# Kernel optimization log

Measured on AMD Instinct MI355X. Metric: run time of the kernel, lower is better.

Reference implementation:

```python
import jax, jax.numpy as jnp
import numpy as np

N_TOKENS = 7168
EMBED_DIM = 256
N_HEADS = 8
HEAD_DIM = EMBED_DIM // N_HEADS  # 32
HALF = HEAD_DIM // 2             # 16 rotary frequency pairs per head
BATCH = 4
MAX_LEN = 2048
POSITION_DIM = 2
N_LEVELS = 4
LN_EPS = 1e-5
SPATIAL_THETA = 100.0
LEVEL_THETA = 10.0


def setup_inputs() -> dict:
    key = jax.random.key(0)
    ks = jax.random.split(key, 6)
    x = jax.random.normal(ks[0], (N_TOKENS, EMBED_DIM), jnp.float32)
    level_indices = jax.random.randint(ks[1], (N_TOKENS,), 0, N_LEVELS, dtype=jnp.int32)
    level_spatial_shapes = jnp.array([[32, 32], [16, 16], [8, 8], [4, 4]], jnp.int32)
    # positions in each token's own level coordinate space
    u = jax.random.uniform(ks[2], (N_TOKENS, POSITION_DIM), jnp.float32)
    spatial_positions = u * level_spatial_shapes[level_indices].astype(jnp.float32)
    # ragged batch boundaries: lengths [2048, 1536, 2048, 1536]
    batch_offsets = jnp.array([0, 2048, 3584, 5632, 7168], jnp.int32)
    ln_w = jnp.ones((EMBED_DIM,), jnp.float32)
    ln_b = jnp.zeros((EMBED_DIM,), jnp.float32)
    qkv_w = jax.random.normal(ks[3], (3 * EMBED_DIM, EMBED_DIM), jnp.float32) * (EMBED_DIM ** -0.5)
    out_w = jax.random.normal(ks[4], (EMBED_DIM, EMBED_DIM), jnp.float32) * (EMBED_DIM ** -0.5)
    # ND-RoPE frequencies: (position_dim+1, n_heads, head_dim//2).
    # Spatial dims share magnitude theta_s^(-i/HALF) split over a random per-head
    # direction angle; level dim uses theta_l^(-i/HALF).
    mag_s = SPATIAL_THETA ** (-jnp.arange(HALF, dtype=jnp.float32) / HALF)
    mag_l = LEVEL_THETA ** (-jnp.arange(HALF, dtype=jnp.float32) / HALF)
    phi = jax.random.uniform(ks[5], (N_HEADS, HALF), jnp.float32) * (2.0 * jnp.pi)
    freqs = jnp.stack([mag_s * jnp.cos(phi),
                       mag_s * jnp.sin(phi),
                       jnp.broadcast_to(mag_l, (N_HEADS, HALF))], axis=0)
    return {"x": x, "spatial_positions": spatial_positions,
            "level_indices": level_indices, "level_spatial_shapes": level_spatial_shapes,
            "batch_offsets": batch_offsets, "ln_w": ln_w, "ln_b": ln_b,
            "qkv_w": qkv_w, "out_w": out_w, "freqs": freqs}


def reference(x, spatial_positions, level_indices, level_spatial_shapes,
              batch_offsets, ln_w, ln_b, qkv_w, out_w, freqs):
    residual = x
    # pre-norm LayerNorm
    mu = jnp.mean(x, -1, keepdims=True)
    var = jnp.mean((x - mu) ** 2, -1, keepdims=True)
    xn = (x - mu) * jax.lax.rsqrt(var + LN_EPS) * ln_w + ln_b
    q, k, v = jnp.split(xn @ qkv_w.T, 3, axis=-1)  # each (N, E)
    # prep_multilevel_positions: rescale each level to the max level's coordinate
    # frame and append the level index as an extra position dim.
    shapes_tok = level_spatial_shapes[level_indices].astype(jnp.float32)  # (N, 2)
    max_shape = jnp.max(level_spatial_shapes, axis=0).astype(jnp.float32)  # (2,)
    pos = jnp.concatenate([spatial_positions * (max_shape / shapes_tok),
                           level_indices[:, None].astype(jnp.float32)], axis=-1)  # (N, 3)
    # per-head ND RoPE: angle = sum_d pos_d * freq_d
    theta = jnp.einsum('nd,dhf->nhf', pos, freqs)  # (N, H, HALF)
    cos, sin = jnp.cos(theta), jnp.sin(theta)

    def rope(t):
        t = t.reshape(N_TOKENS, N_HEADS, HALF, 2)
        r = jnp.stack([t[..., 0] * cos - t[..., 1] * sin,
                       t[..., 0] * sin + t[..., 1] * cos], axis=-1)
        return r.reshape(N_TOKENS, EMBED_DIM)

    q, k = rope(q), rope(k)
    # concatenated -> padded (B, S, E)
    tok = jnp.arange(N_TOKENS)
    b_of = jnp.searchsorted(batch_offsets, tok, side='right') - 1  # (N,) batch index
    p_of = tok - batch_offsets[b_of]                               # (N,) pos in batch
    lens = batch_offsets[1:] - batch_offsets[:-1]
    pad_mask = jnp.arange(MAX_LEN)[None, :] >= lens[:, None]  # (B, S), True = padding

    def heads(t):
        padded = jnp.zeros((BATCH, MAX_LEN, EMBED_DIM), t.dtype).at[b_of, p_of].set(t)
        return padded.reshape(BATCH, MAX_LEN, N_HEADS, HEAD_DIM).transpose(0, 2, 1, 3)

    qh, kh, vh = heads(q), heads(k), heads(v)  # (B, H, S, hd)
    scores = jnp.einsum('bhqd,bhkd->bhqk', qh, kh) / np.float32(np.sqrt(HEAD_DIM))
    scores = jnp.where(pad_mask[:, None, None, :], jnp.float32(-1e9), scores)
    attn = jax.nn.softmax(scores, axis=-1)
    out = jnp.einsum('bhqk,bhkd->bhqd', attn, vh)
    out = out.transpose(0, 2, 1, 3).reshape(BATCH, MAX_LEN, EMBED_DIM)
    out_cat = out[b_of, p_of]  # padded -> concatenated (padded rows dropped)
    return out_cat @ out_w.T + residual
```

## Files before the change

kernel.cpp:

```cpp
#include <hip/hip_runtime.h>
#include <hip/hip_bf16.h>

#define NT   7168
#define ED   256
#define NH   8
#define HD   32
#define HF   16
#define QKVN 768
#define QSCL 0.25503471600819466f

typedef float f32x4  __attribute__((ext_vector_type(4)));
typedef __bf16 bf16x8 __attribute__((ext_vector_type(8)));

__device__ __forceinline__ short f2bf(float f) {
    union { float f; unsigned u; } v; v.f = f;
    unsigned r = v.u + 0x7FFFu + ((v.u >> 16) & 1u);
    return (short)(r >> 16);
}
__device__ __forceinline__ float fexp2(float x) {
    float r; asm("v_exp_f32 %0, %1" : "=v"(r) : "v"(x)); return r;
}
__device__ __forceinline__ unsigned cvtpk(float lo, float hi) {
    unsigned r; asm("v_cvt_pk_bf16_f32 %0, %1, %2" : "=v"(r) : "v"(lo), "v"(hi)); return r;
}
__device__ __forceinline__ float bf2f(short s) {
    union { unsigned u; float f; } v; v.u = ((unsigned)(unsigned short)s) << 16;
    return v.f;
}
__device__ __forceinline__ unsigned pack2bf(float a, float b) {
    union { float f; unsigned u; } ua, ub; ua.f = a; ub.f = b;
    return ((ua.u + 0x8000u) >> 16) | ((ub.u + 0x8000u) & 0xFFFF0000u);
}
__device__ __forceinline__ void gll16(const void* g, void* l) {
    __builtin_amdgcn_global_load_lds((const __attribute__((address_space(1))) void*)g,
                                     (__attribute__((address_space(3))) void*)l, 16, 0, 0);
}

__global__ __launch_bounds__(256) void ln_conv_kernel(const float* __restrict__ x,
                                                      const float* __restrict__ w,
                                                      const float* __restrict__ b,
                                                      short* __restrict__ xn,
                                                      const float* __restrict__ qkvw,
                                                      const float* __restrict__ outw,
                                                      short* __restrict__ wq,
                                                      short* __restrict__ wo,
                                                      const float* __restrict__ sp,
                                                      const int* __restrict__ lvl,
                                                      const int* __restrict__ shp,
                                                      const float* __restrict__ freqs,
                                                      unsigned* __restrict__ tab) {
    int bid = blockIdx.x;
    int tid = threadIdx.x;
    if (bid >= NT / 4) {
        int i = (bid - NT / 4) * 256 + tid;
        if (i < QKVN * ED) wq[i] = f2bf(qkvw[i]);
        if (i < ED * ED)   wo[i] = f2bf(outw[i]);
        return;
    }
    int tok  = bid * 4 + (tid >> 6);
    int lane = tid & 63;
    const float4 xv = *reinterpret_cast<const float4*>(x + tok * ED + lane * 4);
    float s  = xv.x + xv.y + xv.z + xv.w;
    float ss = xv.x * xv.x + xv.y * xv.y + xv.z * xv.z + xv.w * xv.w;
#pragma unroll
    for (int m = 1; m < 64; m <<= 1) { s += __shfl_xor(s, m); ss += __shfl_xor(ss, m); }
    float mu  = s * (1.0f / ED);
    float inv = rsqrtf(ss * (1.0f / ED) - mu * mu + 1e-5f);
    const float4 wv = *reinterpret_cast<const float4*>(w + lane * 4);
    const float4 bv = *reinterpret_cast<const float4*>(b + lane * 4);
    short4 o;
    o.x = f2bf((xv.x - mu) * inv * wv.x + bv.x);
    o.y = f2bf((xv.y - mu) * inv * wv.y + bv.y);
    o.z = f2bf((xv.z - mu) * inv * wv.z + bv.z);
    o.w = f2bf((xv.w - mu) * inv * wv.w + bv.w);
    *reinterpret_cast<short4*>(xn + tok * ED + lane * 4) = o;

    int tt = bid * 4 + (tid >> 6);
    int h  = (tid >> 3) & 7;
    int f  = (tid & 7) * 2;
    int L = lvl[tt];
    float mx0 = fmaxf(fmaxf((float)shp[0], (float)shp[2]), fmaxf((float)shp[4], (float)shp[6]));
    float mx1 = fmaxf(fmaxf((float)shp[1], (float)shp[3]), fmaxf((float)shp[5], (float)shp[7]));
    float p0 = sp[tt * 2]     * (mx0 / (float)shp[L * 2]);
    float p1 = sp[tt * 2 + 1] * (mx1 / (float)shp[L * 2 + 1]);
    float p2 = (float)L;
    int fi = h * HF + f;
    float th0 = p0 * freqs[fi]       + p1 * freqs[128 + fi]       + p2 * freqs[256 + fi];
    float th1 = p0 * freqs[fi + 1]   + p1 * freqs[128 + fi + 1]   + p2 * freqs[256 + fi + 1];
    float sn0, cs0, sn1, cs1;
    __sincosf(th0, &sn0, &cs0);
    __sincosf(th1, &sn1, &cs1);
    uint2 pk;
    pk.x = pack2bf(cs0, sn0);
    pk.y = pack2bf(cs1, sn1);
    *reinterpret_cast<uint2*>(&tab[tt * 128 + fi]) = pk;
}

__global__ __launch_bounds__(256) void gemm_qkv(const short* __restrict__ A,
                                                const short* __restrict__ B,
                                                short* __restrict__ C,
                                                const unsigned* __restrict__ tab,
                                                short* __restrict__ vt) {
    int wv = threadIdx.x >> 6, lane = threadIdx.x & 63;
    int r = lane & 15, g = lane >> 4;
    int mt = blockIdx.x * 128 + wv * 32;
    int jt = blockIdx.y * 64;
    const short* arow0 = A + (mt + r) * ED + g * 8;
    const short* arow1 = A + (mt + 16 + r) * ED + g * 8;
    const short* brow  = B + (jt + r) * ED + g * 8;
    f32x4 acc0[4] = {{0,0,0,0},{0,0,0,0},{0,0,0,0},{0,0,0,0}};
    f32x4 acc1[4] = {{0,0,0,0},{0,0,0,0},{0,0,0,0},{0,0,0,0}};
#pragma unroll
    for (int k0 = 0; k0 < ED; k0 += 32) {
        bf16x8 a0 = *reinterpret_cast<const bf16x8*>(arow0 + k0);
        bf16x8 a1 = *reinterpret_cast<const bf16x8*>(arow1 + k0);
#pragma unroll
        for (int c = 0; c < 4; ++c) {
            bf16x8 bb = *reinterpret_cast<const bf16x8*>(brow + c * 16 * ED + k0);
            acc0[c] = __builtin_amdgcn_mfma_f32_16x16x32_bf16(a0, bb, acc0[c], 0, 0, 0);
            acc1[c] = __builtin_amdgcn_mfma_f32_16x16x32_bf16(a1, bb, acc1[c], 0, 0, 0);
        }
    }
    if (jt < 512) {
        const float qs = (jt < 256) ? QSCL : 1.0f;
        const int sgn = r & 1;
#pragma unroll
        for (int c = 0; c < 4; ++c) {
            int col = jt + c * 16 + r;
            int hf = ((col >> 5) & 7) * 16 + ((col >> 1) & 15);
#pragma unroll
            for (int rr = 0; rr < 4; ++rr) {
                int t0 = mt + g * 4 + rr;
                {
                    unsigned pk = tab[t0 * 128 + hf];
                    float cs = bf2f((short)(pk & 0xFFFF)), sn = bf2f((short)(pk >> 16));
                    float v = acc0[c][rr], p = __shfl_xor(v, 1);
                    float o = sgn ? (v * cs + p * sn) : (v * cs - p * sn);
                    C[t0 * QKVN + col] = f2bf(o * qs);
                }
                {
                    int t1 = t0 + 16;
                    unsigned pk = tab[t1 * 128 + hf];
                    float cs = bf2f((short)(pk & 0xFFFF)), sn = bf2f((short)(pk >> 16));
                    float v = acc1[c][rr], p = __shfl_xor(v, 1);
                    float o = sgn ? (v * cs + p * sn) : (v * cs - p * sn);
                    C[t1 * QKVN + col] = f2bf(o * qs);
                }
            }
        }
    } else {
#pragma unroll
        for (int c = 0; c < 4; ++c) {
            int dg = jt - 512 + c * 16 + r;
#pragma unroll
            for (int rr = 0; rr < 4; ++rr) {
                int t0 = mt + g * 4 + rr;
                int u0 = t0 & 63;
                int s0 = (u0 & 35) | ((u0 & 12) << 1) | ((u0 & 16) >> 2);
                vt[dg * NT + (t0 & ~63) + s0] = f2bf(acc0[c][rr]);
                int t1 = t0 + 16;
                int u1 = t1 & 63;
                int s1 = (u1 & 35) | ((u1 & 12) << 1) | ((u1 & 16) >> 2);
                vt[dg * NT + (t1 & ~63) + s1] = f2bf(acc1[c][rr]);
            }
        }
    }
}

__global__ __launch_bounds__(256) void gemm_out(const short* __restrict__ A,
                                                const short* __restrict__ B,
                                                const float* __restrict__ res,
                                                float* __restrict__ out) {
    int wv = threadIdx.x >> 6, lane = threadIdx.x & 63;
    int r = lane & 15, g = lane >> 4;
    int mt = blockIdx.x * 64 + wv * 16;
    int jt = blockIdx.y * 64;
    const short* arow = A + (mt + r) * ED + g * 8;
    const short* brow = B + (jt + r) * ED + g * 8;
    f32x4 acc[4] = {{0,0,0,0},{0,0,0,0},{0,0,0,0},{0,0,0,0}};
#pragma unroll
    for (int k0 = 0; k0 < ED; k0 += 32) {
        bf16x8 a = *reinterpret_cast<const bf16x8*>(arow + k0);
#pragma unroll
        for (int c = 0; c < 4; ++c) {
            bf16x8 bb = *reinterpret_cast<const bf16x8*>(brow + c * 16 * ED + k0);
            acc[c] = __builtin_amdgcn_mfma_f32_16x16x32_bf16(a, bb, acc[c], 0, 0, 0);
        }
    }
#pragma unroll
    for (int c = 0; c < 4; ++c)
#pragma unroll
        for (int rr = 0; rr < 4; ++rr) {
            int idx = (mt + g * 4 + rr) * ED + jt + c * 16 + r;
            out[idx] = acc[c][rr] + res[idx];
        }
}

__global__ __launch_bounds__(512) void attn_kernel(const short* __restrict__ qkv,
                                                   const short* __restrict__ vt,
                                                   short* __restrict__ obf) {
    __shared__ __align__(16) short smem[16384];
    const int tid = threadIdx.x;
    const int wv = tid >> 6, lane = tid & 63;
    const int bid = blockIdx.x;
    const int h = bid & 7, pr = bid >> 3;
    const int b = (pr >= 16) + (pr >= 28) + (pr >= 44);
    const int off = (b == 0) ? 0 : (b == 1) ? 2048 : (b == 2) ? 3584 : 5632;
    const int len = (b == 0) ? 2048 : (b == 1) ? 1536 : (b == 2) ? 2048 : 1536;
    const int pb  = (b == 0) ? 0 : (b == 1) ? 16 : (b == 2) ? 28 : 44;
    const int q0 = off + (pr - pb) * 128;
    const int r = lane & 15, g = lane >> 4;
    const int qi = wv & 3, half = wv >> 2;
    const int hl = len >> 1;
    const int nst = hl >> 6;
    const int qs = q0 + qi * 32;

    const int shalf = tid >> 8;
    const short* pK = qkv + ED + h * HD + (size_t)(off + ((tid & 255) >> 2)) * QKVN + (tid & 3) * 8;
    const short* pV = vt + (size_t)(h * HD + ((tid >> 2) & 31)) * NT + off + ((tid >> 7) & 1) * 32 + (tid & 3) * 8;
    const int hlK = hl * QKVN;
    const short* pKh = pK + (size_t)shalf * hlK;
    const short* pVh = pV + shalf * hl;

#define STAGE(B, s) { \
        gll16(pKh + (size_t)(s) * 64 * QKVN, &smem[(B) * 8192 +        tid * 8]); \
        gll16(pVh + (s) * 64,                &smem[(B) * 8192 + 4096 + tid * 8]); }

    bf16x8 qfA = *reinterpret_cast<const bf16x8*>(qkv + (size_t)(qs + r) * QKVN + h * HD + g * 8);
    bf16x8 qfB = *reinterpret_cast<const bf16x8*>(qkv + (size_t)(qs + 16 + r) * QKVN + h * HD + g * 8);
    union { unsigned u[4]; bf16x8 v; } onesu;
    onesu.u[0] = onesu.u[1] = onesu.u[2] = onesu.u[3] = 0x3F803F80u;
    const bf16x8 ones = onesu.v;

    f32x4 o0A = {0,0,0,0}, o1A = {0,0,0,0}, o0B = {0,0,0,0}, o1B = {0,0,0,0};
    f32x4 olA = {0,0,0,0}, olB = {0,0,0,0};

    STAGE(0, 0);
    __syncthreads();

    for (int st = 0; st < nst; ++st) {
        const int B = st & 1;
        if (st + 1 < nst) STAGE(B ^ 1, st + 1);
        const short* kl = &smem[B * 8192 + half * 2048];
        const short* vl = &smem[B * 8192 + 4096 + half * 2048];
        bf16x8 kf0 = *reinterpret_cast<const bf16x8*>(kl +        r * 32 + g * 8);
        bf16x8 kf1 = *reinterpret_cast<const bf16x8*>(kl +  512 + r * 32 + g * 8);
        bf16x8 kf2 = *reinterpret_cast<const bf16x8*>(kl + 1024 + r * 32 + g * 8);
        bf16x8 kf3 = *reinterpret_cast<const bf16x8*>(kl + 1536 + r * 32 + g * 8);
        bf16x8 v00 = *reinterpret_cast<const bf16x8*>(vl +        r * 32 + g * 8);
        bf16x8 v10 = *reinterpret_cast<const bf16x8*>(vl +  512 + r * 32 + g * 8);
        bf16x8 v01 = *reinterpret_cast<const bf16x8*>(vl + 1024 + r * 32 + g * 8);
        bf16x8 v11 = *reinterpret_cast<const bf16x8*>(vl + 1536 + r * 32 + g * 8);

        const f32x4 z = {0, 0, 0, 0};
        __builtin_amdgcn_s_setprio(1);
        f32x4 sA0 = __builtin_amdgcn_mfma_f32_16x16x32_bf16(kf0, qfA, z, 0, 0, 0);
        f32x4 sA1 = __builtin_amdgcn_mfma_f32_16x16x32_bf16(kf1, qfA, z, 0, 0, 0);
        f32x4 sA2 = __builtin_amdgcn_mfma_f32_16x16x32_bf16(kf2, qfA, z, 0, 0, 0);
        f32x4 sA3 = __builtin_amdgcn_mfma_f32_16x16x32_bf16(kf3, qfA, z, 0, 0, 0);
        f32x4 sB0 = __builtin_amdgcn_mfma_f32_16x16x32_bf16(kf0, qfB, z, 0, 0, 0);
        f32x4 sB1 = __builtin_amdgcn_mfma_f32_16x16x32_bf16(kf1, qfB, z, 0, 0, 0);
        f32x4 sB2 = __builtin_amdgcn_mfma_f32_16x16x32_bf16(kf2, qfB, z, 0, 0, 0);
        f32x4 sB3 = __builtin_amdgcn_mfma_f32_16x16x32_bf16(kf3, qfB, z, 0, 0, 0);
        __builtin_amdgcn_s_setprio(0);

#pragma unroll
        for (int i = 0; i < 4; ++i) {
            sA0[i] = fexp2(sA0[i]); sA1[i] = fexp2(sA1[i]);
            sA2[i] = fexp2(sA2[i]); sA3[i] = fexp2(sA3[i]);
            sB0[i] = fexp2(sB0[i]); sB1[i] = fexp2(sB1[i]);
            sB2[i] = fexp2(sB2[i]); sB3[i] = fexp2(sB3[i]);
        }
        union { unsigned u[4]; bf16x8 v; } pA0, pA1, pB0, pB1;
        pA0.u[0] = cvtpk(sA0[0], sA0[1]); pA0.u[1] = cvtpk(sA0[2], sA0[3]);
        pA0.u[2] = cvtpk(sA1[0], sA1[1]); pA0.u[3] = cvtpk(sA1[2], sA1[3]);
        pA1.u[0] = cvtpk(sA2[0], sA2[1]); pA1.u[1] = cvtpk(sA2[2], sA2[3]);
        pA1.u[2] = cvtpk(sA3[0], sA3[1]); pA1.u[3] = cvtpk(sA3[2], sA3[3]);
        pB0.u[0] = cvtpk(sB0[0], sB0[1]); pB0.u[1] = cvtpk(sB0[2], sB0[3]);
        pB0.u[2] = cvtpk(sB1[0], sB1[1]); pB0.u[3] = cvtpk(sB1[2], sB1[3]);
        pB1.u[0] = cvtpk(sB2[0], sB2[1]); pB1.u[1] = cvtpk(sB2[2], sB2[3]);
        pB1.u[2] = cvtpk(sB3[0], sB3[1]); pB1.u[3] = cvtpk(sB3[2], sB3[3]);
        __builtin_amdgcn_s_setprio(1);
        o0A = __builtin_amdgcn_mfma_f32_16x16x32_bf16(v00, pA0.v, o0A, 0, 0, 0);
        o0A = __builtin_amdgcn_mfma_f32_16x16x32_bf16(v01, pA1.v, o0A, 0, 0, 0);
        o1A = __builtin_amdgcn_mfma_f32_16x16x32_bf16(v10, pA0.v, o1A, 0, 0, 0);
        o1A = __builtin_amdgcn_mfma_f32_16x16x32_bf16(v11, pA1.v, o1A, 0, 0, 0);
        o0B = __builtin_amdgcn_mfma_f32_16x16x32_bf16(v00, pB0.v, o0B, 0, 0, 0);
        o0B = __builtin_amdgcn_mfma_f32_16x16x32_bf16(v01, pB1.v, o0B, 0, 0, 0);
        o1B = __builtin_amdgcn_mfma_f32_16x16x32_bf16(v10, pB0.v, o1B, 0, 0, 0);
        o1B = __builtin_amdgcn_mfma_f32_16x16x32_bf16(v11, pB1.v, o1B, 0, 0, 0);
        olA = __builtin_amdgcn_mfma_f32_16x16x32_bf16(ones, pA0.v, olA, 0, 0, 0);
        olA = __builtin_amdgcn_mfma_f32_16x16x32_bf16(ones, pA1.v, olA, 0, 0, 0);
        olB = __builtin_amdgcn_mfma_f32_16x16x32_bf16(ones, pB0.v, olB, 0, 0, 0);
        olB = __builtin_amdgcn_mfma_f32_16x16x32_bf16(ones, pB1.v, olB, 0, 0, 0);
        __builtin_amdgcn_s_setprio(0);
        __syncthreads();
    }

    float lA = olA[0], lB = olB[0];

    float* cf = (float*)smem + (qi * 64 + lane) * 19;
    if (half) {
#pragma unroll
        for (int i = 0; i < 4; ++i) {
            cf[i] = o0A[i]; cf[4 + i] = o1A[i]; cf[8 + i] = o0B[i]; cf[12 + i] = o1B[i];
        }
        cf[16] = lA; cf[17] = lB;
    }
    __syncthreads();
    if (!half) {
        lA += cf[16]; lB += cf[17];
#pragma unroll
        for (int i = 0; i < 4; ++i) {
            o0A[i] += cf[i];     o1A[i] += cf[4 + i];
            o0B[i] += cf[8 + i]; o1B[i] += cf[12 + i];
        }
        float iA = 1.f / lA, iB = 1.f / lB;
        short4 w;
        short* orowA = obf + (qs + r) * ED + h * HD;
        w.x = f2bf(o0A[0] * iA); w.y = f2bf(o0A[1] * iA);
        w.z = f2bf(o0A[2] * iA); w.w = f2bf(o0A[3] * iA);
        *reinterpret_cast<short4*>(orowA + g * 4) = w;
        w.x = f2bf(o1A[0] * iA); w.y = f2bf(o1A[1] * iA);
        w.z = f2bf(o1A[2] * iA); w.w = f2bf(o1A[3] * iA);
        *reinterpret_cast<short4*>(orowA + 16 + g * 4) = w;
        short* orowB = obf + (qs + 16 + r) * ED + h * HD;
        w.x = f2bf(o0B[0] * iB); w.y = f2bf(o0B[1] * iB);
        w.z = f2bf(o0B[2] * iB); w.w = f2bf(o0B[3] * iB);
        *reinterpret_cast<short4*>(orowB + g * 4) = w;
        w.x = f2bf(o1B[0] * iB); w.y = f2bf(o1B[1] * iB);
        w.z = f2bf(o1B[2] * iB); w.w = f2bf(o1B[3] * iB);
        *reinterpret_cast<short4*>(orowB + 16 + g * 4) = w;
    }
#undef STAGE
}

extern "C" void kernel_launch(void* const* d_in, const int* in_sizes, int n_in,
                              void* d_out, int out_size, void* d_ws, size_t ws_size,
                              hipStream_t stream) {
    const float* x     = (const float*)d_in[0];
    const float* sp    = (const float*)d_in[1];
    const int*   lvl   = (const int*)d_in[2];
    const int*   shp   = (const int*)d_in[3];
    const float* lnw   = (const float*)d_in[5];
    const float* lnb   = (const float*)d_in[6];
    const float* qkvw  = (const float*)d_in[7];
    const float* outw  = (const float*)d_in[8];
    const float* freqs = (const float*)d_in[9];
    float* out = (float*)d_out;

    char* ws = (char*)d_ws;
    short* xn  = (short*)ws; ws += NT * ED * 2;
    short* qkv = (short*)ws; ws += NT * QKVN * 2;
    short* vt  = (short*)ws; ws += ED * NT * 2;
    short* obf = (short*)ws; ws += NT * ED * 2;
    short* wq  = (short*)ws; ws += QKVN * ED * 2;
    short* wo  = (short*)ws; ws += ED * ED * 2;
    unsigned* tab = (unsigned*)ws; ws += NT * 128 * 4;

    ln_conv_kernel<<<dim3(NT / 4 + 768), dim3(256), 0, stream>>>(
        x, lnw, lnb, xn, qkvw, outw, wq, wo, sp, lvl, shp, freqs, tab);
    gemm_qkv<<<dim3(NT / 128, QKVN / 64), dim3(256), 0, stream>>>(xn, wq, qkv, tab, vt);
    attn_kernel<<<dim3(56 * 8), dim3(512), 0, stream>>>(qkv, vt, obf);
    gemm_out<<<dim3(NT / 64, ED / 64), dim3(256), 0, stream>>>(obf, wo, x, out);
}
```

Before: 67.51 us.

## Split attention key range four ways across 1024-thread blocks

The attention kernel now uses 16 waves per block instead of 8. Each query tile's key sequence is split into four quarters instead of two, with doubled shared memory for staging. The partial outputs and row sums from three waves are reduced through shared memory by the first quarter's wave. This is meant to raise parallelism and cut per-wave loop length, since the grid of 448 blocks is small on a 256-CU part. The cost is a heavier reduction, more shared memory per block, and possible register-pressure limits at 1024 threads.

```diff
diff --git a/kernel.cpp b/kernel.cpp
--- a/kernel.cpp
+++ b/kernel.cpp
@@ -196,10 +196,10 @@
         }
 }
 
-__global__ __launch_bounds__(512) void attn_kernel(const short* __restrict__ qkv,
-                                                   const short* __restrict__ vt,
-                                                   short* __restrict__ obf) {
-    __shared__ __align__(16) short smem[16384];
+__global__ __launch_bounds__(1024) void attn_kernel(const short* __restrict__ qkv,
+                                                    const short* __restrict__ vt,
+                                                    short* __restrict__ obf) {
+    __shared__ __align__(16) short smem[32768];
     const int tid = threadIdx.x;
     const int wv = tid >> 6, lane = tid & 63;
     const int bid = blockIdx.x;
@@ -210,21 +210,19 @@
     const int pb  = (b == 0) ? 0 : (b == 1) ? 16 : (b == 2) ? 28 : 44;
     const int q0 = off + (pr - pb) * 128;
     const int r = lane & 15, g = lane >> 4;
-    const int qi = wv & 3, half = wv >> 2;
-    const int hl = len >> 1;
+    const int qi = wv & 3, qr = wv >> 2;
+    const int hl = len >> 2;
     const int nst = hl >> 6;
     const int qs = q0 + qi * 32;
 
-    const int shalf = tid >> 8;
-    const short* pK = qkv + ED + h * HD + (size_t)(off + ((tid & 255) >> 2)) * QKVN + (tid & 3) * 8;
-    const short* pV = vt + (size_t)(h * HD + ((tid >> 2) & 31)) * NT + off + ((tid >> 7) & 1) * 32 + (tid & 3) * 8;
-    const int hlK = hl * QKVN;
-    const short* pKh = pK + (size_t)shalf * hlK;
-    const short* pVh = pV + shalf * hl;
+    const int qr_s  = tid >> 8;
+    const int inner = tid & 255;
+    const short* pKh = qkv + ED + h * HD + (size_t)(off + qr_s * hl + (inner >> 2)) * QKVN + (inner & 3) * 8;
+    const short* pVh = vt + (size_t)(h * HD + ((inner >> 2) & 31)) * NT + off + qr_s * hl + ((inner >> 7) & 1) * 32 + (inner & 3) * 8;
 
 #define STAGE(B, s) { \
-        gll16(pKh + (size_t)(s) * 64 * QKVN, &smem[(B) * 8192 +        tid * 8]); \
-        gll16(pVh + (s) * 64,                &smem[(B) * 8192 + 4096 + tid * 8]); }
+        gll16(pKh + (size_t)(s) * 64 * QKVN, &smem[(B) * 16384 + qr_s * 4096 +        inner * 8]); \
+        gll16(pVh + (s) * 64,                &smem[(B) * 16384 + qr_s * 4096 + 2048 + inner * 8]); }
 
     bf16x8 qfA = *reinterpret_cast<const bf16x8*>(qkv + (size_t)(qs + r) * QKVN + h * HD + g * 8);
     bf16x8 qfB = *reinterpret_cast<const bf16x8*>(qkv + (size_t)(qs + 16 + r) * QKVN + h * HD + g * 8);
@@ -241,8 +239,8 @@
     for (int st = 0; st < nst; ++st) {
         const int B = st & 1;
         if (st + 1 < nst) STAGE(B ^ 1, st + 1);
-        const short* kl = &smem[B * 8192 + half * 2048];
-        const short* vl = &smem[B * 8192 + 4096 + half * 2048];
+        const short* kl = &smem[B * 16384 + qr * 4096];
+        const short* vl = kl + 2048;
         bf16x8 kf0 = *reinterpret_cast<const bf16x8*>(kl +        r * 32 + g * 8);
         bf16x8 kf1 = *reinterpret_cast<const bf16x8*>(kl +  512 + r * 32 + g * 8);
         bf16x8 kf2 = *reinterpret_cast<const bf16x8*>(kl + 1024 + r * 32 + g * 8);
@@ -299,8 +297,8 @@
 
     float lA = olA[0], lB = olB[0];
 
-    float* cf = (float*)smem + (qi * 64 + lane) * 19;
-    if (half) {
+    if (qr) {
+        float* cf = (float*)smem + ((qi * 3 + (qr - 1)) * 64 + lane) * 18;
 #pragma unroll
         for (int i = 0; i < 4; ++i) {
             cf[i] = o0A[i]; cf[4 + i] = o1A[i]; cf[8 + i] = o0B[i]; cf[12 + i] = o1B[i];
@@ -308,12 +306,16 @@
         cf[16] = lA; cf[17] = lB;
     }
     __syncthreads();
-    if (!half) {
-        lA += cf[16]; lB += cf[17];
-#pragma unroll
-        for (int i = 0; i < 4; ++i) {
-            o0A[i] += cf[i];     o1A[i] += cf[4 + i];
-            o0B[i] += cf[8 + i]; o1B[i] += cf[12 + i];
+    if (qr == 0) {
+#pragma unroll
+        for (int w = 0; w < 3; ++w) {
+            const float* cf = (float*)smem + ((qi * 3 + w) * 64 + lane) * 18;
+            lA += cf[16]; lB += cf[17];
+#pragma unroll
+            for (int i = 0; i < 4; ++i) {
+                o0A[i] += cf[i];     o1A[i] += cf[4 + i];
+                o0B[i] += cf[8 + i]; o1B[i] += cf[12 + i];
+            }
         }
         float iA = 1.f / lA, iB = 1.f / lB;
         short4 w;
@@ -361,6 +363,6 @@
     ln_conv_kernel<<<dim3(NT / 4 + 768), dim3(256), 0, stream>>>(
         x, lnw, lnb, xn, qkvw, outw, wq, wo, sp, lvl, shp, freqs, tab);
     gemm_qkv<<<dim3(NT / 128, QKVN / 64), dim3(256), 0, stream>>>(xn, wq, qkv, tab, vt);
-    attn_kernel<<<dim3(56 * 8), dim3(512), 0, stream>>>(qkv, vt, obf);
+    attn_kernel<<<dim3(56 * 8), dim3(1024), 0, stream>>>(qkv, vt, obf);
     gemm_out<<<dim3(NT / 64, ED / 64), dim3(256), 0, stream>>>(obf, wo, x, out);
 }
```

Result: no change. 68.66 us (+1.7%).
